# Kernel optimization log

Measured on AMD Instinct MI355X. Metric: run time of the kernel, lower is better.

The kernel has to match this reference:

```python
import jax, jax.numpy as jnp
import numpy as np

B, L, D_MODEL, D_K = 4, 2048, 1024, 128


def setup_inputs() -> dict:
    key = jax.random.key(0)
    ks = jax.random.split(key, 4)
    scale = 1.0 / np.sqrt(D_MODEL)
    x = jax.random.normal(ks[0], (B, L, D_MODEL), dtype=jnp.float32)
    Wq = jax.random.normal(ks[1], (D_MODEL, D_K), dtype=jnp.float32) * scale
    Wk = jax.random.normal(ks[2], (D_MODEL, D_K), dtype=jnp.float32) * scale
    Wv = jax.random.normal(ks[3], (D_MODEL, D_K), dtype=jnp.float32) * scale
    bq = jnp.zeros((D_K,), dtype=jnp.float32)
    bk = jnp.zeros((D_K,), dtype=jnp.float32)
    bv = jnp.zeros((D_K,), dtype=jnp.float32)
    return {"x": x, "Wq": Wq, "bq": bq, "Wk": Wk, "bk": bk, "Wv": Wv, "bv": bv}


def reference(x, Wq, bq, Wk, bk, Wv, bv):
    # Dense projections (keras Dense = xW + b)
    Q = jnp.einsum("bld,dk->blk", x, Wq) + bq  # [B, L, d_k]
    K = jnp.einsum("bld,dk->blk", x, Wk) + bk
    V = jnp.einsum("bld,dk->blk", x, Wv) + bv
    QK = jnp.einsum("blk,bmk->blm", Q, K)      # [B, L, L]
    # Original: real( complex(cos(QK), sin(QK)) @ complex(V, 0) )
    # Since imag(V) == 0, the real part is exactly cos(QK) @ V; the sin
    # branch contributes only to the discarded imaginary part.
    out = jnp.einsum("blm,bmk->blk", jnp.cos(QK), V)  # [B, L, d_k]
    return out
```

## Files before the change

kernel.cpp:

```cpp
#include <hip/hip_runtime.h>

typedef _Float16 half8_t __attribute__((ext_vector_type(8)));
typedef __attribute__((ext_vector_type(4))) float float4_t;

#define MFMA16 __builtin_amdgcn_mfma_f32_16x16x32_f16

constexpr int BB   = 4;
constexpr int LL   = 2048;
constexpr int DM   = 1024;
constexpr int DK   = 128;
constexpr int MTOT = BB * LL;
constexpr int MC   = 4;
constexpr float INV2PI = 0.15915494309189535f;


__device__ __forceinline__ void gload16(const void* g, void* l) {
    __builtin_amdgcn_global_load_lds(
        (const __attribute__((address_space(1))) void*)g,
        (__attribute__((address_space(3))) void*)l, 16, 0, 0);
}

__global__ __launch_bounds__(256) void k0_wsplit(
        const float* __restrict__ wq, const float* __restrict__ wk,
        const float* __restrict__ wv,
        _Float16* __restrict__ wq6, _Float16* __restrict__ wk6,
        _Float16* __restrict__ wv6) {
    int kc = blockIdx.x, a = blockIdx.y;
    const float* w = (a == 0) ? wq : (a == 1) ? wk : wv;
    _Float16* dst = (a == 0) ? wq6 : (a == 1) ? wk6 : wv6;
    __shared__ float tile[64 * 132];
    int t = threadIdx.x;
#pragma unroll
    for (int j = 0; j < 8; ++j) {
        int idx4 = t + j * 256;
        int kr = idx4 >> 5, n4 = idx4 & 31;
        *(float4_t*)(&tile[kr * 132 + n4 * 4]) =
            *(const float4_t*)(w + (size_t)(kc * 64 + kr) * DK + n4 * 4);
    }
    __syncthreads();
#pragma unroll
    for (int sw = 0; sw < 4; ++sw) {
        int ch = t + sw * 256;
        int cbt = ch >> 7, s = (ch >> 4) & 7, cc = ch & 15;
        int kb = (s >> 2) * 32 + (s & 3) * 8;
        int n = cbt * 16 + cc;
        half8_t h;
#pragma unroll
        for (int e = 0; e < 8; ++e) h[e] = (_Float16)tile[(kb + e) * 132 + n];
        *(half8_t*)(dst + (size_t)kc * 8192 + ch * 8) = h;
    }
}

__global__ __launch_bounds__(256, 3) void k1_proj(
        const float* __restrict__ x,
        const float* __restrict__ bq, const float* __restrict__ bk,
        const float* __restrict__ bv,
        const _Float16* __restrict__ wq6, const _Float16* __restrict__ wk6,
        const _Float16* __restrict__ wv6,
        _Float16* __restrict__ qim, _Float16* __restrict__ kim,
        _Float16* __restrict__ vim) {
    int mt = blockIdx.x, grp = blockIdx.y;
    int rowbase = mt * 32;
    __shared__ __attribute__((aligned(16))) _Float16 xs[2][32 * 72];
    __shared__ __attribute__((aligned(16))) _Float16 wsm[2][8192];

    int t = threadIdx.x, lane = t & 63, wid = t >> 6;
    int cc = lane & 15, g = lane >> 4;
    const _Float16* W6 = (grp == 0) ? wq6 : (grp == 1) ? wk6 : wv6;

    float4_t acc[2][2];
#pragma unroll
    for (int rf = 0; rf < 2; ++rf)
#pragma unroll
        for (int cf = 0; cf < 2; ++cf) acc[rf][cf] = (float4_t){0.f, 0.f, 0.f, 0.f};

    int xr = t >> 3, xc8 = t & 7;
    const float* xsrc = x + (size_t)(rowbase + xr) * DM + xc8 * 8;
    int xoff = xr * 72 + xc8 * 8;

    auto stageW = [&](int kc, int buf) {
        const _Float16* Wp = W6 + (size_t)kc * 8192;
#pragma unroll
        for (int i = 0; i < 4; ++i)
            gload16(Wp + i * 2048 + t * 8, (char*)wsm[buf] + i * 4096 + wid * 1024);
    };
    auto cvt8 = [&](float4_t f0, float4_t f1) {
        half8_t h;
#pragma unroll
        for (int e = 0; e < 4; ++e) { h[e] = (_Float16)f0[e]; h[e + 4] = (_Float16)f1[e]; }
        return h;
    };

    {
        float4_t f0 = *(const float4_t*)(xsrc);
        float4_t f1 = *(const float4_t*)(xsrc + 4);
        stageW(0, 0);
        *(half8_t*)(xs[0] + xoff) = cvt8(f0, f1);
    }
    __syncthreads();

#pragma unroll 1
    for (int kc = 0; kc < 16; ++kc) {
        int cb = kc & 1, nb = cb ^ 1;
        bool more = (kc < 15);
        float4_t f0, f1;
        if (more) {
            f0 = *(const float4_t*)(xsrc + (size_t)(kc + 1) * 64);
            f1 = *(const float4_t*)(xsrc + (size_t)(kc + 1) * 64 + 4);
            stageW(kc + 1, nb);
        }
        half8_t a_[2][2], b_[2][2];
#pragma unroll
        for (int rf = 0; rf < 2; ++rf)
#pragma unroll
            for (int ks = 0; ks < 2; ++ks)
                a_[rf][ks] = *(const half8_t*)(xs[cb] + (rf * 16 + cc) * 72 + ks * 32 + g * 8);
#pragma unroll
        for (int cf = 0; cf < 2; ++cf)
#pragma unroll
            for (int ks = 0; ks < 2; ++ks)
                b_[cf][ks] = *(const half8_t*)(wsm[cb] + (wid * 2 + cf) * 1024 +
                                               (ks * 4 + g) * 128 + cc * 8);
#pragma unroll
        for (int cf = 0; cf < 2; ++cf)
#pragma unroll
            for (int rf = 0; rf < 2; ++rf) {
                acc[rf][cf] = MFMA16(a_[rf][0], b_[cf][0], acc[rf][cf], 0, 0, 0);
                acc[rf][cf] = MFMA16(a_[rf][1], b_[cf][1], acc[rf][cf], 0, 0, 0);
            }
        if (more) *(half8_t*)(xs[nb] + xoff) = cvt8(f0, f1);
        __syncthreads();
    }

    const float* bias = (grp == 0) ? bq : (grp == 1) ? bk : bv;
#pragma unroll
    for (int rf = 0; rf < 2; ++rf)
#pragma unroll
        for (int cf = 0; cf < 2; ++cf) {
            int c = wid * 32 + cf * 16 + cc;
            float bv_ = bias[c];
#pragma unroll
            for (int i = 0; i < 4; ++i) {
                int r = rowbase + rf * 16 + g * 4 + i;
                float v = acc[rf][cf][i] + bv_;
                if (grp == 0) {
                    size_t o = (size_t)(r >> 4) * 2048 + (c >> 5) * 512 +
                               ((c >> 3) & 3) * 128 + (r & 15) * 8 + (c & 7);
                    qim[o] = (_Float16)v;
                } else if (grp == 1) {
                    size_t o = (size_t)(r >> 5) * 4096 + ((r >> 4) & 1) * 2048 +
                               (c >> 5) * 512 + ((c >> 3) & 3) * 128 +
                               (r & 15) * 8 + (c & 7);
                    kim[o] = (_Float16)v;
                } else {
                    size_t o = (size_t)(r >> 5) * 4096 + (c >> 4) * 512 +
                               ((r >> 3) & 3) * 128 + (c & 15) * 8 + (r & 7);
                    vim[o] = (_Float16)v;
                }
            }
        }
}

__global__ __launch_bounds__(256, 2) void k2_attn(
        const _Float16* __restrict__ qim, const _Float16* __restrict__ kim,
        const _Float16* __restrict__ vim, float* __restrict__ part) {
    int mc = blockIdx.x, qt = blockIdx.y, b = blockIdx.z;
    int t = threadIdx.x, lane = t & 63, wid = t >> 6;
    int cc = lane & 15, g = lane >> 4;

    __shared__ __attribute__((aligned(16))) _Float16 kb[2][8192];
    __shared__ __attribute__((aligned(16))) _Float16 vb[2][8192];
    __shared__ __attribute__((aligned(16))) _Float16 ps[4][1024];

    int qrow = b * LL + qt * 64 + wid * 16;
    const _Float16* qb_ = qim + (size_t)(qrow >> 4) * 2048;
    half8_t qf[4];
#pragma unroll
    for (int s = 0; s < 4; ++s)
        qf[s] = *(const half8_t*)(qb_ + s * 512 + g * 128 + cc * 8);

    float4_t o[8];
#pragma unroll
    for (int cf = 0; cf < 8; ++cf) o[cf] = (float4_t){0.f, 0.f, 0.f, 0.f};

    int tbase = b * 64 + mc * 16;

    auto stageKV = [&](int mi, int buf) {
        const _Float16* ks = kim + (size_t)(tbase + mi * 2) * 4096;
        const _Float16* vs = vim + (size_t)(tbase + mi * 2) * 4096;
#pragma unroll
        for (int i = 0; i < 4; ++i) {
            gload16(ks + i * 2048 + t * 8, (char*)kb[buf] + i * 4096 + wid * 1024);
            gload16(vs + i * 2048 + t * 8, (char*)vb[buf] + i * 4096 + wid * 1024);
        }
    };

    stageKV(0, 0);
    __syncthreads();

#pragma unroll 1
    for (int mi = 0; mi < 8; ++mi) {
        int cb = mi & 1, nb = cb ^ 1;
        if (mi < 7) stageKV(mi + 1, nb);
        float4_t sa[4];
#pragma unroll
        for (int cf = 0; cf < 4; ++cf) sa[cf] = (float4_t){0.f, 0.f, 0.f, 0.f};
#pragma unroll
        for (int cf = 0; cf < 4; ++cf)
#pragma unroll
            for (int s = 0; s < 4; ++s) {
                half8_t bh = *(const half8_t*)(kb[cb] + cf * 2048 + s * 512 +
                                               g * 128 + cc * 8);
                sa[cf] = MFMA16(qf[s], bh, sa[cf], 0, 0, 0);
            }
#pragma unroll
        for (int cf = 0; cf < 4; ++cf)
#pragma unroll
            for (int i = 0; i < 4; ++i) {
                float rv = sa[cf][i] * INV2PI;
                rv = rv - floorf(rv);
                float cv;
                asm volatile("v_cos_f32 %0, %1" : "=v"(cv) : "v"(rv));
                int m = cf * 16 + cc, q = g * 4 + i;
                ps[wid][(m >> 3) * 128 + q * 8 + (m & 7)] = (_Float16)cv;
            }
#pragma unroll
        for (int ksv = 0; ksv < 2; ++ksv) {
            half8_t pa = *(const half8_t*)(&ps[wid][(ksv * 4 + g) * 128 + cc * 8]);
#pragma unroll
            for (int cf = 0; cf < 8; ++cf) {
                half8_t vbf = *(const half8_t*)(vb[cb] + ksv * 4096 + cf * 512 +
                                                g * 128 + cc * 8);
                o[cf] = MFMA16(pa, vbf, o[cf], 0, 0, 0);
            }
        }
        __syncthreads();
    }
    float* pp = part + ((size_t)(mc * BB + b) * LL + qt * 64 + wid * 16) * DK;
#pragma unroll
    for (int cf = 0; cf < 8; ++cf)
#pragma unroll
        for (int i = 0; i < 4; ++i)
            pp[(g * 4 + i) * DK + cf * 16 + cc] = o[cf][i];
}

__global__ __launch_bounds__(256) void k3_reduce(const float4_t* __restrict__ part,
                                                 float4_t* __restrict__ out) {
    constexpr int NT4 = MTOT * DK / 4;
    int idx = blockIdx.x * 256 + threadIdx.x;
    float4_t s = part[idx];
#pragma unroll
    for (int c = 1; c < MC; ++c) s += part[idx + (size_t)c * NT4];
    out[idx] = s;
}

extern "C" void kernel_launch(void* const* d_in, const int* in_sizes, int n_in,
                              void* d_out, int out_size, void* d_ws, size_t ws_size,
                              hipStream_t stream) {
    const float* x  = (const float*)d_in[0];
    const float* Wq = (const float*)d_in[1];
    const float* bq = (const float*)d_in[2];
    const float* Wk = (const float*)d_in[3];
    const float* bk = (const float*)d_in[4];
    const float* Wv = (const float*)d_in[5];
    const float* bv = (const float*)d_in[6];

    char* ws = (char*)d_ws;
    size_t off = 0;
    auto alloc = [&](size_t bytes) -> char* {
        char* p = ws + off;
        off += (bytes + 255) & ~(size_t)255;
        return p;
    };
    _Float16* wq6 = (_Float16*)alloc((size_t)DK * DM * 2);
    _Float16* wk6 = (_Float16*)alloc((size_t)DK * DM * 2);
    _Float16* wv6 = (_Float16*)alloc((size_t)DK * DM * 2);
    _Float16* qim = (_Float16*)alloc((size_t)MTOT * DK * 2);
    _Float16* kim = (_Float16*)alloc((size_t)MTOT * DK * 2);
    _Float16* vim = (_Float16*)alloc((size_t)MTOT * DK * 2);
    float* part = (float*)alloc((size_t)MC * MTOT * DK * 4);

    k0_wsplit<<<dim3(16, 3), 256, 0, stream>>>(Wq, Wk, Wv, wq6, wk6, wv6);
    k1_proj<<<dim3(MTOT / 32, 3), 256, 0, stream>>>(x, bq, bk, bv,
                                                    wq6, wk6, wv6, qim, kim, vim);
    k2_attn<<<dim3(MC, LL / 64, BB), 256, 0, stream>>>(qim, kim, vim, part);
    k3_reduce<<<(MTOT * DK / 4) / 256, 256, 0, stream>>>((const float4_t*)part,
                                                         (float4_t*)d_out);
}
```

Before: 49.45 us.

## Load projection operands directly to registers with software pipelining; pack cos stores

The projection kernel drops LDS staging and barriers. Each wave loads x (fp32) and pre-swizzled fp16 W fragments straight into registers with inline global loads, double-buffered across even and odd k-slices and ordered with explicit vmcnt waits. The block tile grows to 64 rows by 128 columns. In the attention kernel, the QK MFMA operands are swapped so each lane holds four consecutive keys, which lets the cos values be packed with cvt_pkrtz and written to LDS as 32-bit stores instead of scalar half stores. The trade-off is more register pressure, redundant W loads across waves with no LDS sharing, and fragile hand-written waitcnt ordering.

```diff
diff --git a/kernel.cpp b/kernel.cpp
--- a/kernel.cpp
+++ b/kernel.cpp
@@ -1,9 +1,19 @@
 #include <hip/hip_runtime.h>
 
+typedef __attribute__((ext_vector_type(8))) short short8_t;
 typedef _Float16 half8_t __attribute__((ext_vector_type(8)));
+typedef _Float16 half2_t __attribute__((ext_vector_type(2)));
+typedef __fp16 pk2_t __attribute__((ext_vector_type(2)));
+typedef __attribute__((ext_vector_type(4))) int int4_t;
 typedef __attribute__((ext_vector_type(4))) float float4_t;
 
 #define MFMA16 __builtin_amdgcn_mfma_f32_16x16x32_f16
+#define VMCNT(n) asm volatile("s_waitcnt vmcnt(" #n ")" ::: "memory")
+#define SB0 __builtin_amdgcn_sched_barrier(0)
+#define GLOADF4(dst, p) asm volatile("global_load_dwordx4 %0, %1, off" \
+                                     : "=&v"(dst) : "v"(p) : "memory")
+#define GLOADS8(dst, p) asm volatile("global_load_dwordx4 %0, %1, off" \
+                                     : "=&v"(dst) : "v"(p) : "memory")
 
 constexpr int BB   = 4;
 constexpr int LL   = 2048;
@@ -13,11 +23,14 @@
 constexpr int MC   = 4;
 constexpr float INV2PI = 0.15915494309189535f;
 
-
 __device__ __forceinline__ void gload16(const void* g, void* l) {
     __builtin_amdgcn_global_load_lds(
         (const __attribute__((address_space(1))) void*)g,
         (__attribute__((address_space(3))) void*)l, 16, 0, 0);
+}
+__device__ __forceinline__ int pkrtz_i32(float a, float b) {
+    pk2_t p = __builtin_amdgcn_cvt_pkrtz(a, b);
+    return __builtin_bit_cast(int, p);
 }
 
 __global__ __launch_bounds__(256) void k0_wsplit(
@@ -51,7 +64,7 @@
     }
 }
 
-__global__ __launch_bounds__(256, 3) void k1_proj(
+__global__ __launch_bounds__(256) void k1_proj(
         const float* __restrict__ x,
         const float* __restrict__ bq, const float* __restrict__ bk,
         const float* __restrict__ bv,
@@ -60,88 +73,86 @@
         _Float16* __restrict__ qim, _Float16* __restrict__ kim,
         _Float16* __restrict__ vim) {
     int mt = blockIdx.x, grp = blockIdx.y;
-    int rowbase = mt * 32;
-    __shared__ __attribute__((aligned(16))) _Float16 xs[2][32 * 72];
-    __shared__ __attribute__((aligned(16))) _Float16 wsm[2][8192];
-
+    int rowbase = mt * 64;
     int t = threadIdx.x, lane = t & 63, wid = t >> 6;
     int cc = lane & 15, g = lane >> 4;
+    int wrow = (wid >> 1) * 32, wcol = (wid & 1) * 64;
     const _Float16* W6 = (grp == 0) ? wq6 : (grp == 1) ? wk6 : wv6;
 
-    float4_t acc[2][2];
+    float4_t acc[2][4];
 #pragma unroll
     for (int rf = 0; rf < 2; ++rf)
 #pragma unroll
-        for (int cf = 0; cf < 2; ++cf) acc[rf][cf] = (float4_t){0.f, 0.f, 0.f, 0.f};
-
-    int xr = t >> 3, xc8 = t & 7;
-    const float* xsrc = x + (size_t)(rowbase + xr) * DM + xc8 * 8;
-    int xoff = xr * 72 + xc8 * 8;
-
-    auto stageW = [&](int kc, int buf) {
-        const _Float16* Wp = W6 + (size_t)kc * 8192;
-#pragma unroll
-        for (int i = 0; i < 4; ++i)
-            gload16(Wp + i * 2048 + t * 8, (char*)wsm[buf] + i * 4096 + wid * 1024);
+        for (int cf = 0; cf < 4; ++cf) acc[rf][cf] = (float4_t){0.f, 0.f, 0.f, 0.f};
+
+    const float* pA[2];
+#pragma unroll
+    for (int rf = 0; rf < 2; ++rf)
+        pA[rf] = x + (size_t)(rowbase + wrow + rf * 16 + cc) * DM + g * 8;
+    const _Float16* pB[4];
+#pragma unroll
+    for (int cf = 0; cf < 4; ++cf)
+        pB[cf] = W6 + ((wid & 1) * 4 + cf) * 1024 + g * 128 + cc * 8;
+
+    float4_t AE[2][2], AO[2][2];
+    short8_t BE[4], BO[4];
+
+    auto issueSlice = [&](int u, float4_t (&A)[2][2], short8_t (&B)[4]) {
+#pragma unroll
+        for (int rf = 0; rf < 2; ++rf) {
+            const float* p = pA[rf] + u * 32;
+            GLOADF4(A[rf][0], p);
+            GLOADF4(A[rf][1], p + 4);
+        }
+#pragma unroll
+        for (int cf = 0; cf < 4; ++cf) {
+            const _Float16* p = pB[cf] + (u >> 1) * 8192 + (u & 1) * 512;
+            GLOADS8(B[cf], p);
+        }
     };
-    auto cvt8 = [&](float4_t f0, float4_t f1) {
-        half8_t h;
-#pragma unroll
-        for (int e = 0; e < 4; ++e) { h[e] = (_Float16)f0[e]; h[e + 4] = (_Float16)f1[e]; }
-        return h;
+    auto computeAcc = [&](float4_t (&A)[2][2], short8_t (&B)[4]) {
+        half8_t ah[2];
+#pragma unroll
+        for (int rf = 0; rf < 2; ++rf) {
+            int4_t iv;
+#pragma unroll
+            for (int j = 0; j < 4; ++j)
+                iv[j] = pkrtz_i32(A[rf][j >> 1][(j & 1) * 2],
+                                  A[rf][j >> 1][(j & 1) * 2 + 1]);
+            ah[rf] = __builtin_bit_cast(half8_t, iv);
+        }
+#pragma unroll
+        for (int cf = 0; cf < 4; ++cf) {
+            half8_t bh = __builtin_bit_cast(half8_t, B[cf]);
+#pragma unroll
+            for (int rf = 0; rf < 2; ++rf)
+                acc[rf][cf] = MFMA16(ah[rf], bh, acc[rf][cf], 0, 0, 0);
+        }
     };
 
-    {
-        float4_t f0 = *(const float4_t*)(xsrc);
-        float4_t f1 = *(const float4_t*)(xsrc + 4);
-        stageW(0, 0);
-        *(half8_t*)(xs[0] + xoff) = cvt8(f0, f1);
+    issueSlice(0, AE, BE);
+    issueSlice(1, AO, BO);
+#pragma unroll 1
+    for (int u = 0; u < 32; u += 2) {
+        VMCNT(8); SB0;
+        computeAcc(AE, BE);
+        if (u + 2 < 32) issueSlice(u + 2, AE, BE);
+        if (u < 30) { VMCNT(8); } else { VMCNT(0); }
+        SB0;
+        computeAcc(AO, BO);
+        if (u + 3 < 32) issueSlice(u + 3, AO, BO);
     }
-    __syncthreads();
-
-#pragma unroll 1
-    for (int kc = 0; kc < 16; ++kc) {
-        int cb = kc & 1, nb = cb ^ 1;
-        bool more = (kc < 15);
-        float4_t f0, f1;
-        if (more) {
-            f0 = *(const float4_t*)(xsrc + (size_t)(kc + 1) * 64);
-            f1 = *(const float4_t*)(xsrc + (size_t)(kc + 1) * 64 + 4);
-            stageW(kc + 1, nb);
-        }
-        half8_t a_[2][2], b_[2][2];
-#pragma unroll
-        for (int rf = 0; rf < 2; ++rf)
-#pragma unroll
-            for (int ks = 0; ks < 2; ++ks)
-                a_[rf][ks] = *(const half8_t*)(xs[cb] + (rf * 16 + cc) * 72 + ks * 32 + g * 8);
-#pragma unroll
-        for (int cf = 0; cf < 2; ++cf)
-#pragma unroll
-            for (int ks = 0; ks < 2; ++ks)
-                b_[cf][ks] = *(const half8_t*)(wsm[cb] + (wid * 2 + cf) * 1024 +
-                                               (ks * 4 + g) * 128 + cc * 8);
-#pragma unroll
-        for (int cf = 0; cf < 2; ++cf)
-#pragma unroll
-            for (int rf = 0; rf < 2; ++rf) {
-                acc[rf][cf] = MFMA16(a_[rf][0], b_[cf][0], acc[rf][cf], 0, 0, 0);
-                acc[rf][cf] = MFMA16(a_[rf][1], b_[cf][1], acc[rf][cf], 0, 0, 0);
-            }
-        if (more) *(half8_t*)(xs[nb] + xoff) = cvt8(f0, f1);
-        __syncthreads();
-    }
 
     const float* bias = (grp == 0) ? bq : (grp == 1) ? bk : bv;
 #pragma unroll
     for (int rf = 0; rf < 2; ++rf)
 #pragma unroll
-        for (int cf = 0; cf < 2; ++cf) {
-            int c = wid * 32 + cf * 16 + cc;
+        for (int cf = 0; cf < 4; ++cf) {
+            int c = wcol + cf * 16 + cc;
             float bv_ = bias[c];
 #pragma unroll
             for (int i = 0; i < 4; ++i) {
-                int r = rowbase + rf * 16 + g * 4 + i;
+                int r = rowbase + wrow + rf * 16 + g * 4 + i;
                 float v = acc[rf][cf][i] + bv_;
                 if (grp == 0) {
                     size_t o = (size_t)(r >> 4) * 2048 + (c >> 5) * 512 +
@@ -209,21 +220,25 @@
         for (int cf = 0; cf < 4; ++cf)
 #pragma unroll
             for (int s = 0; s < 4; ++s) {
-                half8_t bh = *(const half8_t*)(kb[cb] + cf * 2048 + s * 512 +
+                half8_t kf = *(const half8_t*)(kb[cb] + cf * 2048 + s * 512 +
                                                g * 128 + cc * 8);
-                sa[cf] = MFMA16(qf[s], bh, sa[cf], 0, 0, 0);
+                sa[cf] = MFMA16(kf, qf[s], sa[cf], 0, 0, 0);
             }
 #pragma unroll
-        for (int cf = 0; cf < 4; ++cf)
+        for (int cf = 0; cf < 4; ++cf) {
+            float cv[4];
 #pragma unroll
             for (int i = 0; i < 4; ++i) {
                 float rv = sa[cf][i] * INV2PI;
                 rv = rv - floorf(rv);
-                float cv;
-                asm volatile("v_cos_f32 %0, %1" : "=v"(cv) : "v"(rv));
-                int m = cf * 16 + cc, q = g * 4 + i;
-                ps[wid][(m >> 3) * 128 + q * 8 + (m & 7)] = (_Float16)cv;
+                asm volatile("v_cos_f32 %0, %1" : "=v"(cv[i]) : "v"(rv));
             }
+            int p0 = pkrtz_i32(cv[0], cv[1]);
+            int p1 = pkrtz_i32(cv[2], cv[3]);
+            int base = (2 * cf + (g >> 1)) * 128 + cc * 8 + (g & 1) * 4;
+            *(int*)(&ps[wid][base])     = p0;
+            *(int*)(&ps[wid][base + 2]) = p1;
+        }
 #pragma unroll
         for (int ksv = 0; ksv < 2; ++ksv) {
             half8_t pa = *(const half8_t*)(&ps[wid][(ksv * 4 + g) * 128 + cc * 8]);
@@ -281,7 +296,7 @@
     float* part = (float*)alloc((size_t)MC * MTOT * DK * 4);
 
     k0_wsplit<<<dim3(16, 3), 256, 0, stream>>>(Wq, Wk, Wv, wq6, wk6, wv6);
-    k1_proj<<<dim3(MTOT / 32, 3), 256, 0, stream>>>(x, bq, bk, bv,
+    k1_proj<<<dim3(MTOT / 64, 3), 256, 0, stream>>>(x, bq, bk, bv,
                                                     wq6, wk6, wv6, qim, kim, vim);
     k2_attn<<<dim3(MC, LL / 64, BB), 256, 0, stream>>>(qim, kim, vim, part);
     k3_reduce<<<(MTOT * DK / 4) / 256, 256, 0, stream>>>((const float4_t*)part,
```

After: 70.40 us. +42.4%, slower.

## Double row tiles in projection and attention kernels to reuse staged K/V and W

Applied to the files above, without the earlier changes.

The projection kernel now handles 64 rows per block, with a 2x2 warp layout where each warp computes 32 rows by 64 columns, so every staged weight chunk serves twice as many rows. The attention kernel now gives each warp two 16-row query tiles, so each K and V fragment loaded from LDS feeds two MFMAs. It also swaps the QK^T operand order so the cosine results can be written to LDS as packed half2 stores. The cost is more registers per thread, dropped occupancy hints, and half as many blocks, which lowers parallelism on the large CU count.

```diff
diff --git a/kernel.cpp b/kernel.cpp
--- a/kernel.cpp
+++ b/kernel.cpp
@@ -1,6 +1,7 @@
 #include <hip/hip_runtime.h>
 
 typedef _Float16 half8_t __attribute__((ext_vector_type(8)));
+typedef _Float16 half2_t __attribute__((ext_vector_type(2)));
 typedef __attribute__((ext_vector_type(4))) float float4_t;
 
 #define MFMA16 __builtin_amdgcn_mfma_f32_16x16x32_f16
@@ -12,7 +13,6 @@
 constexpr int MTOT = BB * LL;
 constexpr int MC   = 4;
 constexpr float INV2PI = 0.15915494309189535f;
-
 
 __device__ __forceinline__ void gload16(const void* g, void* l) {
     __builtin_amdgcn_global_load_lds(
@@ -51,7 +51,7 @@
     }
 }
 
-__global__ __launch_bounds__(256, 3) void k1_proj(
+__global__ __launch_bounds__(256) void k1_proj(
         const float* __restrict__ x,
         const float* __restrict__ bq, const float* __restrict__ bk,
         const float* __restrict__ bv,
@@ -60,23 +60,27 @@
         _Float16* __restrict__ qim, _Float16* __restrict__ kim,
         _Float16* __restrict__ vim) {
     int mt = blockIdx.x, grp = blockIdx.y;
-    int rowbase = mt * 32;
-    __shared__ __attribute__((aligned(16))) _Float16 xs[2][32 * 72];
+    int rowbase = mt * 64;
+    __shared__ __attribute__((aligned(16))) _Float16 xs[2][64 * 72];
     __shared__ __attribute__((aligned(16))) _Float16 wsm[2][8192];
 
     int t = threadIdx.x, lane = t & 63, wid = t >> 6;
     int cc = lane & 15, g = lane >> 4;
+    int wr = (wid >> 1) * 32;
+    int wcN = wid & 1;
     const _Float16* W6 = (grp == 0) ? wq6 : (grp == 1) ? wk6 : wv6;
 
-    float4_t acc[2][2];
+    float4_t acc[2][4];
 #pragma unroll
     for (int rf = 0; rf < 2; ++rf)
 #pragma unroll
-        for (int cf = 0; cf < 2; ++cf) acc[rf][cf] = (float4_t){0.f, 0.f, 0.f, 0.f};
-
-    int xr = t >> 3, xc8 = t & 7;
-    const float* xsrc = x + (size_t)(rowbase + xr) * DM + xc8 * 8;
-    int xoff = xr * 72 + xc8 * 8;
+        for (int cf = 0; cf < 4; ++cf) acc[rf][cf] = (float4_t){0.f, 0.f, 0.f, 0.f};
+
+    int xrow = t >> 3, xc8 = t & 7;
+    const float* xsrc0 = x + (size_t)(rowbase + xrow) * DM + xc8 * 8;
+    const float* xsrc1 = xsrc0 + (size_t)32 * DM;
+    int xo0 = xrow * 72 + xc8 * 8;
+    int xo1 = (xrow + 32) * 72 + xc8 * 8;
 
     auto stageW = [&](int kc, int buf) {
         const _Float16* Wp = W6 + (size_t)kc * 8192;
@@ -92,10 +96,11 @@
     };
 
     {
-        float4_t f0 = *(const float4_t*)(xsrc);
-        float4_t f1 = *(const float4_t*)(xsrc + 4);
+        float4_t a0 = *(const float4_t*)(xsrc0), a1 = *(const float4_t*)(xsrc0 + 4);
+        float4_t b0 = *(const float4_t*)(xsrc1), b1 = *(const float4_t*)(xsrc1 + 4);
         stageW(0, 0);
-        *(half8_t*)(xs[0] + xoff) = cvt8(f0, f1);
+        *(half8_t*)(xs[0] + xo0) = cvt8(a0, a1);
+        *(half8_t*)(xs[0] + xo1) = cvt8(b0, b1);
     }
     __syncthreads();
 
@@ -103,32 +108,38 @@
     for (int kc = 0; kc < 16; ++kc) {
         int cb = kc & 1, nb = cb ^ 1;
         bool more = (kc < 15);
-        float4_t f0, f1;
+        float4_t a0, a1, b0, b1;
         if (more) {
-            f0 = *(const float4_t*)(xsrc + (size_t)(kc + 1) * 64);
-            f1 = *(const float4_t*)(xsrc + (size_t)(kc + 1) * 64 + 4);
+            a0 = *(const float4_t*)(xsrc0 + (size_t)(kc + 1) * 64);
+            a1 = *(const float4_t*)(xsrc0 + (size_t)(kc + 1) * 64 + 4);
+            b0 = *(const float4_t*)(xsrc1 + (size_t)(kc + 1) * 64);
+            b1 = *(const float4_t*)(xsrc1 + (size_t)(kc + 1) * 64 + 4);
             stageW(kc + 1, nb);
         }
-        half8_t a_[2][2], b_[2][2];
+        half8_t a_[2][2], b_[4][2];
 #pragma unroll
         for (int rf = 0; rf < 2; ++rf)
 #pragma unroll
             for (int ks = 0; ks < 2; ++ks)
-                a_[rf][ks] = *(const half8_t*)(xs[cb] + (rf * 16 + cc) * 72 + ks * 32 + g * 8);
-#pragma unroll
-        for (int cf = 0; cf < 2; ++cf)
+                a_[rf][ks] = *(const half8_t*)(xs[cb] + (wr + rf * 16 + cc) * 72 +
+                                               ks * 32 + g * 8);
+#pragma unroll
+        for (int cf = 0; cf < 4; ++cf)
 #pragma unroll
             for (int ks = 0; ks < 2; ++ks)
-                b_[cf][ks] = *(const half8_t*)(wsm[cb] + (wid * 2 + cf) * 1024 +
+                b_[cf][ks] = *(const half8_t*)(wsm[cb] + (wcN * 4 + cf) * 1024 +
                                                (ks * 4 + g) * 128 + cc * 8);
 #pragma unroll
-        for (int cf = 0; cf < 2; ++cf)
+        for (int cf = 0; cf < 4; ++cf)
 #pragma unroll
             for (int rf = 0; rf < 2; ++rf) {
                 acc[rf][cf] = MFMA16(a_[rf][0], b_[cf][0], acc[rf][cf], 0, 0, 0);
                 acc[rf][cf] = MFMA16(a_[rf][1], b_[cf][1], acc[rf][cf], 0, 0, 0);
             }
-        if (more) *(half8_t*)(xs[nb] + xoff) = cvt8(f0, f1);
+        if (more) {
+            *(half8_t*)(xs[nb] + xo0) = cvt8(a0, a1);
+            *(half8_t*)(xs[nb] + xo1) = cvt8(b0, b1);
+        }
         __syncthreads();
     }
 
@@ -136,12 +147,12 @@
 #pragma unroll
     for (int rf = 0; rf < 2; ++rf)
 #pragma unroll
-        for (int cf = 0; cf < 2; ++cf) {
-            int c = wid * 32 + cf * 16 + cc;
+        for (int cf = 0; cf < 4; ++cf) {
+            int c = wcN * 64 + cf * 16 + cc;
             float bv_ = bias[c];
 #pragma unroll
             for (int i = 0; i < 4; ++i) {
-                int r = rowbase + rf * 16 + g * 4 + i;
+                int r = rowbase + wr + rf * 16 + g * 4 + i;
                 float v = acc[rf][cf][i] + bv_;
                 if (grp == 0) {
                     size_t o = (size_t)(r >> 4) * 2048 + (c >> 5) * 512 +
@@ -161,7 +172,7 @@
         }
 }
 
-__global__ __launch_bounds__(256, 2) void k2_attn(
+__global__ __launch_bounds__(256) void k2_attn(
         const _Float16* __restrict__ qim, const _Float16* __restrict__ kim,
         const _Float16* __restrict__ vim, float* __restrict__ part) {
     int mc = blockIdx.x, qt = blockIdx.y, b = blockIdx.z;
@@ -170,18 +181,22 @@
 
     __shared__ __attribute__((aligned(16))) _Float16 kb[2][8192];
     __shared__ __attribute__((aligned(16))) _Float16 vb[2][8192];
-    __shared__ __attribute__((aligned(16))) _Float16 ps[4][1024];
-
-    int qrow = b * LL + qt * 64 + wid * 16;
-    const _Float16* qb_ = qim + (size_t)(qrow >> 4) * 2048;
-    half8_t qf[4];
-#pragma unroll
-    for (int s = 0; s < 4; ++s)
-        qf[s] = *(const half8_t*)(qb_ + s * 512 + g * 128 + cc * 8);
-
-    float4_t o[8];
-#pragma unroll
-    for (int cf = 0; cf < 8; ++cf) o[cf] = (float4_t){0.f, 0.f, 0.f, 0.f};
+    __shared__ __attribute__((aligned(16))) _Float16 ps[4][2][1024];
+
+    int qrow0 = b * LL + qt * 128 + wid * 32;
+    half8_t qf[2][4];
+#pragma unroll
+    for (int qti = 0; qti < 2; ++qti) {
+        const _Float16* qb_ = qim + (size_t)((qrow0 + qti * 16) >> 4) * 2048;
+#pragma unroll
+        for (int s = 0; s < 4; ++s)
+            qf[qti][s] = *(const half8_t*)(qb_ + s * 512 + g * 128 + cc * 8);
+    }
+    float4_t o[2][8];
+#pragma unroll
+    for (int qti = 0; qti < 2; ++qti)
+#pragma unroll
+        for (int cf = 0; cf < 8; ++cf) o[qti][cf] = (float4_t){0.f, 0.f, 0.f, 0.f};
 
     int tbase = b * 64 + mc * 16;
 
@@ -202,46 +217,64 @@
     for (int mi = 0; mi < 8; ++mi) {
         int cb = mi & 1, nb = cb ^ 1;
         if (mi < 7) stageKV(mi + 1, nb);
-        float4_t sa[4];
-#pragma unroll
-        for (int cf = 0; cf < 4; ++cf) sa[cf] = (float4_t){0.f, 0.f, 0.f, 0.f};
+        float4_t sa[2][4];
+#pragma unroll
+        for (int qti = 0; qti < 2; ++qti)
+#pragma unroll
+            for (int cf = 0; cf < 4; ++cf) sa[qti][cf] = (float4_t){0.f, 0.f, 0.f, 0.f};
 #pragma unroll
         for (int cf = 0; cf < 4; ++cf)
 #pragma unroll
             for (int s = 0; s < 4; ++s) {
-                half8_t bh = *(const half8_t*)(kb[cb] + cf * 2048 + s * 512 +
+                half8_t kf = *(const half8_t*)(kb[cb] + cf * 2048 + s * 512 +
                                                g * 128 + cc * 8);
-                sa[cf] = MFMA16(qf[s], bh, sa[cf], 0, 0, 0);
-            }
-#pragma unroll
-        for (int cf = 0; cf < 4; ++cf)
-#pragma unroll
-            for (int i = 0; i < 4; ++i) {
-                float rv = sa[cf][i] * INV2PI;
-                rv = rv - floorf(rv);
-                float cv;
-                asm volatile("v_cos_f32 %0, %1" : "=v"(cv) : "v"(rv));
-                int m = cf * 16 + cc, q = g * 4 + i;
-                ps[wid][(m >> 3) * 128 + q * 8 + (m & 7)] = (_Float16)cv;
+                sa[0][cf] = MFMA16(kf, qf[0][s], sa[0][cf], 0, 0, 0);
+                sa[1][cf] = MFMA16(kf, qf[1][s], sa[1][cf], 0, 0, 0);
+            }
+#pragma unroll
+        for (int qti = 0; qti < 2; ++qti)
+#pragma unroll
+            for (int cf = 0; cf < 4; ++cf) {
+                float cv[4];
+#pragma unroll
+                for (int i = 0; i < 4; ++i) {
+                    float rv = sa[qti][cf][i] * INV2PI;
+                    rv = rv - floorf(rv);
+                    asm volatile("v_cos_f32 %0, %1" : "=v"(cv[i]) : "v"(rv));
+                }
+                int base = (2 * cf + (g >> 1)) * 128 + cc * 8 + (g & 1) * 4;
+                half2_t h01 = {(_Float16)cv[0], (_Float16)cv[1]};
+                half2_t h23 = {(_Float16)cv[2], (_Float16)cv[3]};
+                *(half2_t*)(&ps[wid][qti][base])     = h01;
+                *(half2_t*)(&ps[wid][qti][base + 2]) = h23;
             }
 #pragma unroll
         for (int ksv = 0; ksv < 2; ++ksv) {
-            half8_t pa = *(const half8_t*)(&ps[wid][(ksv * 4 + g) * 128 + cc * 8]);
-#pragma unroll
-            for (int cf = 0; cf < 8; ++cf) {
-                half8_t vbf = *(const half8_t*)(vb[cb] + ksv * 4096 + cf * 512 +
-                                                g * 128 + cc * 8);
-                o[cf] = MFMA16(pa, vbf, o[cf], 0, 0, 0);
+            half8_t vf[8];
+#pragma unroll
+            for (int cf = 0; cf < 8; ++cf)
+                vf[cf] = *(const half8_t*)(vb[cb] + ksv * 4096 + cf * 512 +
+                                           g * 128 + cc * 8);
+#pragma unroll
+            for (int qti = 0; qti < 2; ++qti) {
+                half8_t pa = *(const half8_t*)(&ps[wid][qti][(ksv * 4 + g) * 128 + cc * 8]);
+#pragma unroll
+                for (int cf = 0; cf < 8; ++cf)
+                    o[qti][cf] = MFMA16(pa, vf[cf], o[qti][cf], 0, 0, 0);
             }
         }
         __syncthreads();
     }
-    float* pp = part + ((size_t)(mc * BB + b) * LL + qt * 64 + wid * 16) * DK;
-#pragma unroll
-    for (int cf = 0; cf < 8; ++cf)
-#pragma unroll
-        for (int i = 0; i < 4; ++i)
-            pp[(g * 4 + i) * DK + cf * 16 + cc] = o[cf][i];
+#pragma unroll
+    for (int qti = 0; qti < 2; ++qti) {
+        float* pp = part + ((size_t)(mc * BB + b) * LL + qt * 128 + wid * 32 +
+                            qti * 16) * DK;
+#pragma unroll
+        for (int cf = 0; cf < 8; ++cf)
+#pragma unroll
+            for (int i = 0; i < 4; ++i)
+                pp[(g * 4 + i) * DK + cf * 16 + cc] = o[qti][cf][i];
+    }
 }
 
 __global__ __launch_bounds__(256) void k3_reduce(const float4_t* __restrict__ part,
@@ -281,9 +314,9 @@
     float* part = (float*)alloc((size_t)MC * MTOT * DK * 4);
 
     k0_wsplit<<<dim3(16, 3), 256, 0, stream>>>(Wq, Wk, Wv, wq6, wk6, wv6);
-    k1_proj<<<dim3(MTOT / 32, 3), 256, 0, stream>>>(x, bq, bk, bv,
+    k1_proj<<<dim3(MTOT / 64, 3), 256, 0, stream>>>(x, bq, bk, bv,
                                                     wq6, wk6, wv6, qim, kim, vim);
-    k2_attn<<<dim3(MC, LL / 64, BB), 256, 0, stream>>>(qim, kim, vim, part);
+    k2_attn<<<dim3(MC, LL / 128, BB), 256, 0, stream>>>(qim, kim, vim, part);
     k3_reduce<<<(MTOT * DK / 4) / 256, 256, 0, stream>>>((const float4_t*)part,
                                                          (float4_t*)d_out);
 }
```

Result: slower. 54.05 us (+9.3%).

## Give each attention wave two query tiles and split keys into eight chunks

Applied to the files above, without the earlier changes.

Each wave now owns 32 query rows (two 16-row tiles) and reuses every K and V fragment loaded from LDS for both tiles. The key dimension is split into 8 chunks instead of 4, and each iteration stages a single 32-key tile. QK^T is computed with the operands swapped so the cos results pack into half4 LDS stores. The aim is to halve LDS reads per MFMA and shrink shared memory per block. In exchange, the partial-sum buffer and the reduce kernel's traffic double, register use rises, and the occupancy hint in launch bounds is dropped.

```diff
diff --git a/kernel.cpp b/kernel.cpp
--- a/kernel.cpp
+++ b/kernel.cpp
@@ -1,6 +1,7 @@
 #include <hip/hip_runtime.h>
 
 typedef _Float16 half8_t __attribute__((ext_vector_type(8)));
+typedef _Float16 half4_t __attribute__((ext_vector_type(4)));
 typedef __attribute__((ext_vector_type(4))) float float4_t;
 
 #define MFMA16 __builtin_amdgcn_mfma_f32_16x16x32_f16
@@ -10,9 +11,8 @@
 constexpr int DM   = 1024;
 constexpr int DK   = 128;
 constexpr int MTOT = BB * LL;
-constexpr int MC   = 4;
+constexpr int MC   = 8;
 constexpr float INV2PI = 0.15915494309189535f;
-
 
 __device__ __forceinline__ void gload16(const void* g, void* l) {
     __builtin_amdgcn_global_load_lds(
@@ -161,35 +161,39 @@
         }
 }
 
-__global__ __launch_bounds__(256, 2) void k2_attn(
+__global__ __launch_bounds__(256) void k2_attn(
         const _Float16* __restrict__ qim, const _Float16* __restrict__ kim,
         const _Float16* __restrict__ vim, float* __restrict__ part) {
     int mc = blockIdx.x, qt = blockIdx.y, b = blockIdx.z;
     int t = threadIdx.x, lane = t & 63, wid = t >> 6;
     int cc = lane & 15, g = lane >> 4;
 
-    __shared__ __attribute__((aligned(16))) _Float16 kb[2][8192];
-    __shared__ __attribute__((aligned(16))) _Float16 vb[2][8192];
-    __shared__ __attribute__((aligned(16))) _Float16 ps[4][1024];
-
-    int qrow = b * LL + qt * 64 + wid * 16;
-    const _Float16* qb_ = qim + (size_t)(qrow >> 4) * 2048;
-    half8_t qf[4];
-#pragma unroll
-    for (int s = 0; s < 4; ++s)
-        qf[s] = *(const half8_t*)(qb_ + s * 512 + g * 128 + cc * 8);
-
-    float4_t o[8];
-#pragma unroll
-    for (int cf = 0; cf < 8; ++cf) o[cf] = (float4_t){0.f, 0.f, 0.f, 0.f};
-
-    int tbase = b * 64 + mc * 16;
+    __shared__ __attribute__((aligned(16))) _Float16 kb[2][4096];
+    __shared__ __attribute__((aligned(16))) _Float16 vb[2][4096];
+    __shared__ __attribute__((aligned(16))) _Float16 ps[4][2][512];
+
+    int qrow0 = b * LL + qt * 128 + wid * 32;
+    half8_t qf[2][4];
+#pragma unroll
+    for (int qti = 0; qti < 2; ++qti) {
+        const _Float16* qb_ = qim + (size_t)((qrow0 + qti * 16) >> 4) * 2048;
+#pragma unroll
+        for (int s = 0; s < 4; ++s)
+            qf[qti][s] = *(const half8_t*)(qb_ + s * 512 + g * 128 + cc * 8);
+    }
+    float4_t o[2][8];
+#pragma unroll
+    for (int qti = 0; qti < 2; ++qti)
+#pragma unroll
+        for (int cf = 0; cf < 8; ++cf) o[qti][cf] = (float4_t){0.f, 0.f, 0.f, 0.f};
+
+    int tbase = b * 64 + mc * 8;
 
     auto stageKV = [&](int mi, int buf) {
-        const _Float16* ks = kim + (size_t)(tbase + mi * 2) * 4096;
-        const _Float16* vs = vim + (size_t)(tbase + mi * 2) * 4096;
-#pragma unroll
-        for (int i = 0; i < 4; ++i) {
+        const _Float16* ks = kim + (size_t)(tbase + mi) * 4096;
+        const _Float16* vs = vim + (size_t)(tbase + mi) * 4096;
+#pragma unroll
+        for (int i = 0; i < 2; ++i) {
             gload16(ks + i * 2048 + t * 8, (char*)kb[buf] + i * 4096 + wid * 1024);
             gload16(vs + i * 2048 + t * 8, (char*)vb[buf] + i * 4096 + wid * 1024);
         }
@@ -202,46 +206,56 @@
     for (int mi = 0; mi < 8; ++mi) {
         int cb = mi & 1, nb = cb ^ 1;
         if (mi < 7) stageKV(mi + 1, nb);
-        float4_t sa[4];
-#pragma unroll
-        for (int cf = 0; cf < 4; ++cf) sa[cf] = (float4_t){0.f, 0.f, 0.f, 0.f};
-#pragma unroll
-        for (int cf = 0; cf < 4; ++cf)
+        float4_t sa[2][2];
+#pragma unroll
+        for (int qti = 0; qti < 2; ++qti)
+#pragma unroll
+            for (int cf = 0; cf < 2; ++cf) sa[qti][cf] = (float4_t){0.f, 0.f, 0.f, 0.f};
+#pragma unroll
+        for (int cf = 0; cf < 2; ++cf)
 #pragma unroll
             for (int s = 0; s < 4; ++s) {
-                half8_t bh = *(const half8_t*)(kb[cb] + cf * 2048 + s * 512 +
+                half8_t kf = *(const half8_t*)(kb[cb] + cf * 2048 + s * 512 +
                                                g * 128 + cc * 8);
-                sa[cf] = MFMA16(qf[s], bh, sa[cf], 0, 0, 0);
+                sa[0][cf] = MFMA16(kf, qf[0][s], sa[0][cf], 0, 0, 0);
+                sa[1][cf] = MFMA16(kf, qf[1][s], sa[1][cf], 0, 0, 0);
             }
 #pragma unroll
-        for (int cf = 0; cf < 4; ++cf)
-#pragma unroll
-            for (int i = 0; i < 4; ++i) {
-                float rv = sa[cf][i] * INV2PI;
-                rv = rv - floorf(rv);
-                float cv;
-                asm volatile("v_cos_f32 %0, %1" : "=v"(cv) : "v"(rv));
-                int m = cf * 16 + cc, q = g * 4 + i;
-                ps[wid][(m >> 3) * 128 + q * 8 + (m & 7)] = (_Float16)cv;
+        for (int qti = 0; qti < 2; ++qti)
+#pragma unroll
+            for (int cf = 0; cf < 2; ++cf) {
+                half4_t h4;
+#pragma unroll
+                for (int i = 0; i < 4; ++i) {
+                    float rv = sa[qti][cf][i] * INV2PI;
+                    rv = rv - floorf(rv);
+                    float cv;
+                    asm volatile("v_cos_f32 %0, %1" : "=v"(cv) : "v"(rv));
+                    h4[i] = (_Float16)cv;
+                }
+                int base = (cf * 2 + (g >> 1)) * 128 + cc * 8 + (g & 1) * 4;
+                *(half4_t*)(&ps[wid][qti][base]) = h4;
             }
-#pragma unroll
-        for (int ksv = 0; ksv < 2; ++ksv) {
-            half8_t pa = *(const half8_t*)(&ps[wid][(ksv * 4 + g) * 128 + cc * 8]);
-#pragma unroll
-            for (int cf = 0; cf < 8; ++cf) {
-                half8_t vbf = *(const half8_t*)(vb[cb] + ksv * 4096 + cf * 512 +
-                                                g * 128 + cc * 8);
-                o[cf] = MFMA16(pa, vbf, o[cf], 0, 0, 0);
-            }
+        half8_t pa0 = *(const half8_t*)(&ps[wid][0][g * 128 + cc * 8]);
+        half8_t pa1 = *(const half8_t*)(&ps[wid][1][g * 128 + cc * 8]);
+#pragma unroll
+        for (int cf = 0; cf < 8; ++cf) {
+            half8_t vf = *(const half8_t*)(vb[cb] + cf * 512 + g * 128 + cc * 8);
+            o[0][cf] = MFMA16(pa0, vf, o[0][cf], 0, 0, 0);
+            o[1][cf] = MFMA16(pa1, vf, o[1][cf], 0, 0, 0);
         }
         __syncthreads();
     }
-    float* pp = part + ((size_t)(mc * BB + b) * LL + qt * 64 + wid * 16) * DK;
-#pragma unroll
-    for (int cf = 0; cf < 8; ++cf)
-#pragma unroll
-        for (int i = 0; i < 4; ++i)
-            pp[(g * 4 + i) * DK + cf * 16 + cc] = o[cf][i];
+#pragma unroll
+    for (int qti = 0; qti < 2; ++qti) {
+        float* pp = part + ((size_t)(mc * BB + b) * LL + qt * 128 + wid * 32 +
+                            qti * 16) * DK;
+#pragma unroll
+        for (int cf = 0; cf < 8; ++cf)
+#pragma unroll
+            for (int i = 0; i < 4; ++i)
+                pp[(g * 4 + i) * DK + cf * 16 + cc] = o[qti][cf][i];
+    }
 }
 
 __global__ __launch_bounds__(256) void k3_reduce(const float4_t* __restrict__ part,
@@ -283,7 +297,7 @@
     k0_wsplit<<<dim3(16, 3), 256, 0, stream>>>(Wq, Wk, Wv, wq6, wk6, wv6);
     k1_proj<<<dim3(MTOT / 32, 3), 256, 0, stream>>>(x, bq, bk, bv,
                                                     wq6, wk6, wv6, qim, kim, vim);
-    k2_attn<<<dim3(MC, LL / 64, BB), 256, 0, stream>>>(qim, kim, vim, part);
+    k2_attn<<<dim3(MC, LL / 128, BB), 256, 0, stream>>>(qim, kim, vim, part);
     k3_reduce<<<(MTOT * DK / 4) / 256, 256, 0, stream>>>((const float4_t*)part,
                                                          (float4_t*)d_out);
 }
```

Result: slower. 52.11 us (+5.4%).
